# Optimization experiments

Hardware: AMD Instinct MI355X
Metric: run time of the kernel (lower is better)

The kernel has to match this reference:

```python
import jax, jax.numpy as jnp
import numpy as np

N = 100000       # num_nodes
E = 1600000      # num_edges (avg degree 16)
EL = 200000      # link-prediction edges
IN_C = 64
POS = 16
HID = 64
OUT = 32


def setup_inputs() -> dict:
    key = jax.random.key(0)
    ks = jax.random.split(key, 10)
    def glorot(k, shape):
        scale = 1.0 / np.sqrt(shape[0])
        return jax.random.uniform(k, shape, jnp.float32, -scale, scale)
    return {
        "x": jax.random.normal(ks[0], (N, IN_C), jnp.float32),
        "pos_emb": jax.random.normal(ks[1], (N, POS), jnp.float32),
        "W1": glorot(ks[2], (IN_C + POS, HID)),
        "b1": jnp.zeros((HID,), jnp.float32),
        "W2": glorot(ks[3], (HID, OUT)),
        "b2": jnp.zeros((OUT,), jnp.float32),
        "Wl": glorot(ks[4], (2 * OUT, 1)),
        "bl": jnp.zeros((1,), jnp.float32),
        "edge_index": jax.random.randint(ks[5], (2, E), 0, N, jnp.int32),
        "edge_label_index": jax.random.randint(ks[6], (2, EL), 0, N, jnp.int32),
    }


def reference(x, pos_emb, W1, b1, W2, b2, Wl, bl, edge_index, edge_label_index):
    n = x.shape[0]
    # GCNConv: add self-loops, symmetric deg^{-1/2} normalization (PyG defaults)
    loops = jnp.arange(n, dtype=edge_index.dtype)
    src = jnp.concatenate([edge_index[0], loops])  # [E+N]
    dst = jnp.concatenate([edge_index[1], loops])  # [E+N]
    deg = jax.ops.segment_sum(jnp.ones_like(dst, jnp.float32), dst, num_segments=n)
    dinv = jnp.where(deg > 0, jax.lax.rsqrt(jnp.maximum(deg, 1e-12)), 0.0)
    norm = dinv[src] * dinv[dst]  # [E+N]

    def gcn_conv(h, W, b):
        hw = h @ W                                    # [N, d_out] transform first
        msg = hw[src] * norm[:, None]                 # gather + normalize
        return jax.ops.segment_sum(msg, dst, num_segments=n) + b  # scatter-add

    h = jnp.concatenate([x, pos_emb], axis=1)         # [N, in+pos]
    h = jax.nn.relu(gcn_conv(h, W1, b1))              # dropout is eval no-op
    z = gcn_conv(h, W2, b2)                           # [N, out]

    s, d = edge_label_index[0], edge_label_index[1]
    zc = jnp.concatenate([z[s], z[d]], axis=1)        # [EL, 2*out]
    edge_pred = (zc @ Wl + bl)[:, 0]                  # [EL]
    return z, edge_pred
```

## Files before the change

kernel.cpp:

```cpp
#include <hip/hip_runtime.h>
#include <hip/hip_fp16.h>

#define NN 100000
#define NE 1600000
#define NEL 200000
#define TM 64

#define NBUCK 196
#define CAPB  10240
#define TPE   8192

typedef short s16x8 __attribute__((ext_vector_type(8)));
typedef float f32x4 __attribute__((ext_vector_type(4)));

__device__ __forceinline__ unsigned short bf16hi(float v) {
    unsigned u = __float_as_uint(v);
    return (unsigned short)((u + 0x7FFFu + ((u >> 16) & 1u)) >> 16);
}
__device__ __forceinline__ float bf16tof(unsigned short b) {
    return __uint_as_float(((unsigned)b) << 16);
}

__global__ __launch_bounds__(256) void k_part(const int* __restrict__ src,
                                              const int* __restrict__ dst,
                                              int* __restrict__ gcur,
                                              int* __restrict__ part) {
    __shared__ int hist[NBUCK];
    __shared__ int base[NBUCK];
    __shared__ int rk[NBUCK];
    int tid = threadIdx.x;
    for (int i = tid; i < NBUCK; i += 256) { hist[i] = 0; rk[i] = 0; }
    __syncthreads();
    int e0 = blockIdx.x * TPE;
    int e1 = min(e0 + TPE, NE);
    for (int e = e0 + tid; e < e1; e += 256)
        atomicAdd(&hist[dst[e] >> 9], 1);
    __syncthreads();
    for (int i = tid; i < NBUCK; i += 256)
        base[i] = i * CAPB + atomicAdd(&gcur[i], hist[i]);
    __syncthreads();
    for (int e = e0 + tid; e < e1; e += 256) {
        int d = dst[e];
        int s = src[e];
        int b = d >> 9;
        int r = atomicAdd(&rk[b], 1);
        part[base[b] + r] = ((d & 511) << 17) | s;
    }
}

__global__ __launch_bounds__(256) void k_build(const int* __restrict__ gcur,
                                               const int* __restrict__ part,
                                               int* __restrict__ csr,
                                               int* __restrict__ off,
                                               float* __restrict__ dinv) {
    __shared__ int cnts[256];
    __shared__ int hist[512];
    __shared__ int loff[512];
    __shared__ int ssum[256];
    __shared__ int csrbuf[CAPB];
    int b = blockIdx.x;
    int tid = threadIdx.x;
    cnts[tid] = (tid < NBUCK) ? gcur[tid] : 0;
    __syncthreads();
    for (int st = 1; st < 256; st <<= 1) {
        int tmp = (tid >= st) ? cnts[tid - st] : 0;
        __syncthreads();
        cnts[tid] += tmp;
        __syncthreads();
    }
    int obase = (b == 0) ? 0 : cnts[b - 1];
    int cnt = gcur[b];
    int pbase = b * CAPB;
    hist[tid] = 0; hist[tid + 256] = 0;
    __syncthreads();
    for (int i = tid; i < cnt; i += 256)
        atomicAdd(&hist[part[pbase + i] >> 17], 1);
    __syncthreads();
    int a0 = hist[2 * tid], a1 = hist[2 * tid + 1];
    int pairs = a0 + a1;
    ssum[tid] = pairs;
    __syncthreads();
    for (int st = 1; st < 256; st <<= 1) {
        int tmp = (tid >= st) ? ssum[tid - st] : 0;
        __syncthreads();
        ssum[tid] += tmp;
        __syncthreads();
    }
    int pexcl = ssum[tid] - pairs;
    loff[2 * tid] = pexcl;
    loff[2 * tid + 1] = pexcl + a0;
    __syncthreads();
    for (int i = tid; i < 512; i += 256) {
        int d = b * 512 + i;
        if (d < NN) {
            int c = hist[i];
            off[d] = obase + loff[i] + c;
            dinv[d] = rsqrtf((float)(c + 1));
        }
    }
    hist[tid] = 0; hist[tid + 256] = 0;
    __syncthreads();
    for (int i = tid; i < cnt; i += 256) {
        int rec = part[pbase + i];
        int dl = rec >> 17;
        int r = atomicAdd(&hist[dl], 1);
        csrbuf[loff[dl] + r] = rec & 0x1FFFF;
    }
    __syncthreads();
    for (int i = tid; i < cnt; i += 256)
        csr[obase + i] = csrbuf[i];
}

#define HW1_K 104
__global__ __launch_bounds__(256) void k_hw1(const float* __restrict__ x,
                                             const float* __restrict__ pos,
                                             const float* __restrict__ W1,
                                             const float* __restrict__ dinv,
                                             __half* __restrict__ hw1) {
    __shared__ unsigned short ahi[64 * HW1_K];
    __shared__ unsigned short alo[64 * HW1_K];
    __shared__ unsigned short bhi[64 * HW1_K];
    __shared__ unsigned short blo[64 * HW1_K];
    __shared__ float sdin[64];
    int tid = threadIdx.x;
    int nb = blockIdx.x * 64;
    for (int i = tid; i < 64 * 24; i += 256) {
        int r = i / 24, c = i - r * 24;
        ahi[r * HW1_K + 80 + c] = 0; alo[r * HW1_K + 80 + c] = 0;
        bhi[r * HW1_K + 80 + c] = 0; blo[r * HW1_K + 80 + c] = 0;
    }
    for (int i = tid; i < 64 * 64; i += 256) {
        int r = i >> 6, c = i & 63;
        int g = nb + r;
        float v = (g < NN) ? x[g * 64 + c] : 0.0f;
        unsigned short h = bf16hi(v);
        ahi[r * HW1_K + c] = h;
        alo[r * HW1_K + c] = bf16hi(v - bf16tof(h));
    }
    for (int i = tid; i < 64 * 16; i += 256) {
        int r = i >> 4, c = i & 15;
        int g = nb + r;
        float v = (g < NN) ? pos[g * 16 + c] : 0.0f;
        unsigned short h = bf16hi(v);
        ahi[r * HW1_K + 64 + c] = h;
        alo[r * HW1_K + 64 + c] = bf16hi(v - bf16tof(h));
    }
    for (int i = tid; i < 80 * 64; i += 256) {
        int k = i >> 6, c = i & 63;
        float v = W1[i];
        unsigned short h = bf16hi(v);
        bhi[c * HW1_K + k] = h;
        blo[c * HW1_K + k] = bf16hi(v - bf16tof(h));
    }
    for (int i = tid; i < 64; i += 256) {
        int g = nb + i;
        sdin[i] = (g < NN) ? dinv[g] : 0.0f;
    }
    __syncthreads();
    int wave = tid >> 6, lane = tid & 63;
    int frow = lane & 15, fq = lane >> 4;
    int r0 = wave * 16;
    int aoff = (r0 + frow) * HW1_K + fq * 8;
    s16x8 ah0 = *(s16x8*)&ahi[aoff];
    s16x8 ah1 = *(s16x8*)&ahi[aoff + 32];
    s16x8 ah2 = *(s16x8*)&ahi[aoff + 64];
    s16x8 al0 = *(s16x8*)&alo[aoff];
    s16x8 al1 = *(s16x8*)&alo[aoff + 32];
    s16x8 al2 = *(s16x8*)&alo[aoff + 64];
    f32x4 acc[4];
#pragma unroll
    for (int ct = 0; ct < 4; ++ct) {
        acc[ct] = (f32x4)(0.0f);
        int boff = (ct * 16 + frow) * HW1_K + fq * 8;
        s16x8 bh0 = *(s16x8*)&bhi[boff];
        s16x8 bh1 = *(s16x8*)&bhi[boff + 32];
        s16x8 bh2 = *(s16x8*)&bhi[boff + 64];
        s16x8 bl0 = *(s16x8*)&blo[boff];
        s16x8 bl1 = *(s16x8*)&blo[boff + 32];
        s16x8 bl2 = *(s16x8*)&blo[boff + 64];
        acc[ct] = __builtin_amdgcn_mfma_f32_16x16x32_bf16(ah0, bh0, acc[ct], 0, 0, 0);
        acc[ct] = __builtin_amdgcn_mfma_f32_16x16x32_bf16(ah1, bh1, acc[ct], 0, 0, 0);
        acc[ct] = __builtin_amdgcn_mfma_f32_16x16x32_bf16(ah2, bh2, acc[ct], 0, 0, 0);
        acc[ct] = __builtin_amdgcn_mfma_f32_16x16x32_bf16(ah0, bl0, acc[ct], 0, 0, 0);
        acc[ct] = __builtin_amdgcn_mfma_f32_16x16x32_bf16(ah1, bl1, acc[ct], 0, 0, 0);
        acc[ct] = __builtin_amdgcn_mfma_f32_16x16x32_bf16(ah2, bl2, acc[ct], 0, 0, 0);
        acc[ct] = __builtin_amdgcn_mfma_f32_16x16x32_bf16(al0, bh0, acc[ct], 0, 0, 0);
        acc[ct] = __builtin_amdgcn_mfma_f32_16x16x32_bf16(al1, bh1, acc[ct], 0, 0, 0);
        acc[ct] = __builtin_amdgcn_mfma_f32_16x16x32_bf16(al2, bh2, acc[ct], 0, 0, 0);
    }
#pragma unroll
    for (int ct = 0; ct < 4; ++ct) {
        int col = ct * 16 + frow;
#pragma unroll
        for (int i = 0; i < 4; ++i) {
            int r = r0 + fq * 4 + i;
            int g = nb + r;
            if (g < NN)
                hw1[g * 64 + col] = __float2half_rn(acc[ct][i] * sdin[r]);
        }
    }
}

__global__ __launch_bounds__(256) void k_gather1(const int* __restrict__ off,
                                                 const int* __restrict__ csr,
                                                 const float* __restrict__ dinv,
                                                 const __half* __restrict__ hw,
                                                 const float* __restrict__ b1,
                                                 const float* __restrict__ W2,
                                                 __half* __restrict__ hw2out) {
    __shared__ float sW2[64 * 32];
    __shared__ float h2row[4][64];
    int tid = threadIdx.x;
    for (int t = tid; t < 64 * 32; t += 256) sW2[t] = W2[t];
    int lane = tid & 63;
    int wave = tid >> 6;
    int d = blockIdx.x * 4 + wave;
    int start = (d == 0) ? 0 : off[d - 1];
    int end = off[d];
    start = __builtin_amdgcn_readfirstlane(start);
    end   = __builtin_amdgcn_readfirstlane(end);
    float dd = dinv[d];
    float hself = __half2float(hw[d * 64 + lane]);
    __syncthreads();
    float acc0 = 0.0f, acc1 = 0.0f, acc2 = 0.0f, acc3 = 0.0f;
    for (int e = start; e < end; e += 16) {
        int rem = end - e;
        int s0 = csr[e];
        int s1  = (rem > 1)  ? csr[e + 1]  : s0;
        int s2  = (rem > 2)  ? csr[e + 2]  : s0;
        int s3  = (rem > 3)  ? csr[e + 3]  : s0;
        int s4  = (rem > 4)  ? csr[e + 4]  : s0;
        int s5  = (rem > 5)  ? csr[e + 5]  : s0;
        int s6  = (rem > 6)  ? csr[e + 6]  : s0;
        int s7  = (rem > 7)  ? csr[e + 7]  : s0;
        int s8  = (rem > 8)  ? csr[e + 8]  : s0;
        int s9  = (rem > 9)  ? csr[e + 9]  : s0;
        int s10 = (rem > 10) ? csr[e + 10] : s0;
        int s11 = (rem > 11) ? csr[e + 11] : s0;
        int s12 = (rem > 12) ? csr[e + 12] : s0;
        int s13 = (rem > 13) ? csr[e + 13] : s0;
        int s14 = (rem > 14) ? csr[e + 14] : s0;
        int s15 = (rem > 15) ? csr[e + 15] : s0;
        float g0  = __half2float(hw[s0  * 64 + lane]);
        float g1  = __half2float(hw[s1  * 64 + lane]);
        float g2  = __half2float(hw[s2  * 64 + lane]);
        float g3  = __half2float(hw[s3  * 64 + lane]);
        float g4  = __half2float(hw[s4  * 64 + lane]);
        float g5  = __half2float(hw[s5  * 64 + lane]);
        float g6  = __half2float(hw[s6  * 64 + lane]);
        float g7  = __half2float(hw[s7  * 64 + lane]);
        float g8  = __half2float(hw[s8  * 64 + lane]);
        float g9  = __half2float(hw[s9  * 64 + lane]);
        float g10 = __half2float(hw[s10 * 64 + lane]);
        float g11 = __half2float(hw[s11 * 64 + lane]);
        float g12 = __half2float(hw[s12 * 64 + lane]);
        float g13 = __half2float(hw[s13 * 64 + lane]);
        float g14 = __half2float(hw[s14 * 64 + lane]);
        float g15 = __half2float(hw[s15 * 64 + lane]);
        int inv = 16 - rem;
        if (inv < 0) inv = 0;
        acc0 += g0;  acc1 += g1;  acc2 += g2;  acc3 += g3;
        acc0 += g4;  acc1 += g5;  acc2 += g6;  acc3 += g7;
        acc0 += g8;  acc1 += g9;  acc2 += g10; acc3 += g11;
        acc0 += g12; acc1 += g13; acc2 += g14; acc3 += g15;
        acc3 = fmaf(-(float)inv, g0, acc3);
    }
    float v = fmaxf(b1[lane] + dd * (((acc0 + acc1) + (acc2 + acc3)) + hself), 0.0f);
    h2row[wave][lane] = v;
    int j = lane & 31;
    int half = lane >> 5;
    float sum = 0.0f;
#pragma unroll
    for (int k = 0; k < 32; ++k) {
        int kk = half * 32 + k;
        sum += h2row[wave][kk] * sW2[kk * 32 + j];
    }
    sum += __shfl_xor(sum, 32, 64);
    if (half == 0)
        hw2out[d * 32 + j] = __float2half_rn(sum * dd);
}

__global__ __launch_bounds__(256) void k_gather2(const int* __restrict__ off,
                                                 const int* __restrict__ csr,
                                                 const float* __restrict__ dinv,
                                                 const __half* __restrict__ hw,
                                                 const float* __restrict__ b2,
                                                 const float* __restrict__ Wl,
                                                 float* __restrict__ outz,
                                                 float* __restrict__ uu,
                                                 float* __restrict__ vv) {
    int lane = threadIdx.x & 63;
    int half = lane >> 5;
    int j = lane & 31;
    int wave = threadIdx.x >> 6;
    int d = blockIdx.x * 4 + wave;
    int start = (d == 0) ? 0 : off[d - 1];
    int end = off[d];
    start = __builtin_amdgcn_readfirstlane(start);
    end   = __builtin_amdgcn_readfirstlane(end);
    float dd = dinv[d];
    float hself = __half2float(hw[d * 32 + j]);
    float accA = 0.0f, accB = 0.0f, accC = 0.0f, accD = 0.0f;
    for (int e = start; e < end; e += 16) {
        int rem = end - e;
        int s0 = csr[e];
        int i1 = e + half;
        int sA = (half      < rem) ? csr[i1]      : s0;
        int sB = (half + 2  < rem) ? csr[i1 + 2]  : s0;
        int sC = (half + 4  < rem) ? csr[i1 + 4]  : s0;
        int sD = (half + 6  < rem) ? csr[i1 + 6]  : s0;
        int sE = (half + 8  < rem) ? csr[i1 + 8]  : s0;
        int sF = (half + 10 < rem) ? csr[i1 + 10] : s0;
        int sG = (half + 12 < rem) ? csr[i1 + 12] : s0;
        int sH = (half + 14 < rem) ? csr[i1 + 14] : s0;
        float gA = __half2float(hw[sA * 32 + j]);
        float gB = __half2float(hw[sB * 32 + j]);
        float gC = __half2float(hw[sC * 32 + j]);
        float gD = __half2float(hw[sD * 32 + j]);
        float gE = __half2float(hw[sE * 32 + j]);
        float gF = __half2float(hw[sF * 32 + j]);
        float gG = __half2float(hw[sG * 32 + j]);
        float gH = __half2float(hw[sH * 32 + j]);
        int nv = (rem - half + 1) >> 1;
        if (nv > 8) nv = 8;
        int inv = 8 - nv;
        accA += gA; accB += gB; accC += gC; accD += gD;
        accA += gE; accB += gF; accC += gG; accD += gH;
        accD = fmaf(-(float)inv, gH, accD);
    }
    float acc = (accA + accB) + (accC + accD);
    acc += __shfl(acc, lane ^ 32, 64);
    float z = b2[j] + dd * (acc + hself);
    if (half == 0)
        outz[d * 32 + j] = z;
    float p0 = z * Wl[j];
    float p1 = z * Wl[32 + j];
    p0 += __shfl_xor(p0, 1, 64);  p1 += __shfl_xor(p1, 1, 64);
    p0 += __shfl_xor(p0, 2, 64);  p1 += __shfl_xor(p1, 2, 64);
    p0 += __shfl_xor(p0, 4, 64);  p1 += __shfl_xor(p1, 4, 64);
    p0 += __shfl_xor(p0, 8, 64);  p1 += __shfl_xor(p1, 8, 64);
    p0 += __shfl_xor(p0, 16, 64); p1 += __shfl_xor(p1, 16, 64);
    if (lane == 0) { uu[d] = p0; vv[d] = p1; }
}

__global__ __launch_bounds__(256) void k_linkpred(const int* __restrict__ sidx,
                                                  const int* __restrict__ didx,
                                                  const float* __restrict__ uu,
                                                  const float* __restrict__ vv,
                                                  const float* __restrict__ bl,
                                                  float* __restrict__ pred) {
    int e = blockIdx.x * 256 + threadIdx.x;
    if (e < NEL)
        pred[e] = uu[sidx[e]] + vv[didx[e]] + bl[0];
}

extern "C" void kernel_launch(void* const* d_in, const int* in_sizes, int n_in,
                              void* d_out, int out_size, void* d_ws, size_t ws_size,
                              hipStream_t stream) {
    const float* x    = (const float*)d_in[0];
    const float* pos  = (const float*)d_in[1];
    const float* W1   = (const float*)d_in[2];
    const float* b1   = (const float*)d_in[3];
    const float* W2   = (const float*)d_in[4];
    const float* b2   = (const float*)d_in[5];
    const float* Wl   = (const float*)d_in[6];
    const float* bl   = (const float*)d_in[7];
    const int*   ei   = (const int*)d_in[8];
    const int*   eli  = (const int*)d_in[9];
    const int* src  = ei;
    const int* dst  = ei + NE;
    const int* lsrc = eli;
    const int* ldst = eli + NEL;

    float* out_z    = (float*)d_out;
    float* out_pred = (float*)d_out + NN * 32;

    float*  dinv  = (float*)d_ws;
    int*    off   = (int*)(dinv + NN);
    int*    gcur  = off + NN;
    int*    csr   = gcur + NBUCK;
    __half* hw1   = (__half*)(csr + NE);
    int*    part  = (int*)hw1;
    __half* hw2   = hw1 + NN * 64;
    float*  uu    = (float*)(hw2 + NN * 32);
    float*  vv    = uu + NN;

    hipMemsetAsync(gcur, 0, NBUCK * sizeof(int), stream);
    k_part<<<(NE + TPE - 1) / TPE, 256, 0, stream>>>(src, dst, gcur, part);
    k_build<<<NBUCK, 256, 0, stream>>>(gcur, part, csr, off, dinv);

    k_hw1<<<(NN + TM - 1) / TM, 256, 0, stream>>>(x, pos, W1, dinv, hw1);

    k_gather1<<<NN / 4, 256, 0, stream>>>(off, csr, dinv, hw1, b1, W2, hw2);

    k_gather2<<<NN / 4, 256, 0, stream>>>(off, csr, dinv, hw2, b2, Wl,
                                          out_z, uu, vv);

    k_linkpred<<<(NEL + 255) / 256, 256, 0, stream>>>(lsrc, ldst, uu, vv, bl,
                                                      out_pred);
}
```

Measured before the change: 280.2 us.

## Fuse CSR partition and build kernels via grid-wide atomic barrier

Merges the partition and bucket-build kernels into one 196-block kernel that uses a global atomic counter as a grid barrier, removing one launch and its inter-kernel gap. Shared memory is unioned between the two phases. It also drops staging W2 into shared memory in the first gather kernel and reads it directly from global, which removes a block-wide sync. The grid barrier depends on all 196 blocks being co-resident, which holds on a GPU with enough CUs but would deadlock otherwise.

```diff
diff --git a/kernel.cpp b/kernel.cpp
--- a/kernel.cpp
+++ b/kernel.cpp
@@ -9,6 +9,7 @@
 #define NBUCK 196
 #define CAPB  10240
 #define TPE   8192
+#define NPART 196
 
 typedef short s16x8 __attribute__((ext_vector_type(8)));
 typedef float f32x4 __attribute__((ext_vector_type(4)));
@@ -21,94 +22,96 @@
     return __uint_as_float(((unsigned)b) << 16);
 }
 
-__global__ __launch_bounds__(256) void k_part(const int* __restrict__ src,
-                                              const int* __restrict__ dst,
-                                              int* __restrict__ gcur,
-                                              int* __restrict__ part) {
-    __shared__ int hist[NBUCK];
-    __shared__ int base[NBUCK];
-    __shared__ int rk[NBUCK];
+union CsrSmem {
+    struct { int hist[NBUCK], base[NBUCK], rk[NBUCK]; } p;
+    struct { int cnts[256], hist[512], loff[512], ssum[256], csrbuf[CAPB]; } b;
+};
+__global__ __launch_bounds__(256) void k_csr(const int* __restrict__ src,
+                                             const int* __restrict__ dst,
+                                             int* __restrict__ gcur,
+                                             int* __restrict__ bar,
+                                             int* __restrict__ part,
+                                             int* __restrict__ csr,
+                                             int* __restrict__ off,
+                                             float* __restrict__ dinv) {
+    __shared__ CsrSmem sm;
     int tid = threadIdx.x;
-    for (int i = tid; i < NBUCK; i += 256) { hist[i] = 0; rk[i] = 0; }
-    __syncthreads();
-    int e0 = blockIdx.x * TPE;
+    int b = blockIdx.x;
+    for (int i = tid; i < NBUCK; i += 256) { sm.p.hist[i] = 0; sm.p.rk[i] = 0; }
+    __syncthreads();
+    int e0 = b * TPE;
     int e1 = min(e0 + TPE, NE);
     for (int e = e0 + tid; e < e1; e += 256)
-        atomicAdd(&hist[dst[e] >> 9], 1);
+        atomicAdd(&sm.p.hist[dst[e] >> 9], 1);
     __syncthreads();
     for (int i = tid; i < NBUCK; i += 256)
-        base[i] = i * CAPB + atomicAdd(&gcur[i], hist[i]);
+        sm.p.base[i] = i * CAPB + atomicAdd(&gcur[i], sm.p.hist[i]);
     __syncthreads();
     for (int e = e0 + tid; e < e1; e += 256) {
         int d = dst[e];
         int s = src[e];
-        int b = d >> 9;
-        int r = atomicAdd(&rk[b], 1);
-        part[base[b] + r] = ((d & 511) << 17) | s;
-    }
-}
-
-__global__ __launch_bounds__(256) void k_build(const int* __restrict__ gcur,
-                                               const int* __restrict__ part,
-                                               int* __restrict__ csr,
-                                               int* __restrict__ off,
-                                               float* __restrict__ dinv) {
-    __shared__ int cnts[256];
-    __shared__ int hist[512];
-    __shared__ int loff[512];
-    __shared__ int ssum[256];
-    __shared__ int csrbuf[CAPB];
-    int b = blockIdx.x;
-    int tid = threadIdx.x;
-    cnts[tid] = (tid < NBUCK) ? gcur[tid] : 0;
+        int bk = d >> 9;
+        int r = atomicAdd(&sm.p.rk[bk], 1);
+        part[sm.p.base[bk] + r] = ((d & 511) << 17) | s;
+    }
+    __syncthreads();
+    if (tid == 0) {
+        __threadfence();
+        __hip_atomic_fetch_add(bar, 1, __ATOMIC_RELEASE, __HIP_MEMORY_SCOPE_AGENT);
+        while (__hip_atomic_load(bar, __ATOMIC_ACQUIRE, __HIP_MEMORY_SCOPE_AGENT) < NPART)
+            __builtin_amdgcn_s_sleep(16);
+        __threadfence();
+    }
+    __syncthreads();
+    sm.b.cnts[tid] = (tid < NBUCK) ? gcur[tid] : 0;
     __syncthreads();
     for (int st = 1; st < 256; st <<= 1) {
-        int tmp = (tid >= st) ? cnts[tid - st] : 0;
+        int tmp = (tid >= st) ? sm.b.cnts[tid - st] : 0;
         __syncthreads();
-        cnts[tid] += tmp;
+        sm.b.cnts[tid] += tmp;
         __syncthreads();
     }
-    int obase = (b == 0) ? 0 : cnts[b - 1];
+    int obase = (b == 0) ? 0 : sm.b.cnts[b - 1];
     int cnt = gcur[b];
     int pbase = b * CAPB;
-    hist[tid] = 0; hist[tid + 256] = 0;
+    sm.b.hist[tid] = 0; sm.b.hist[tid + 256] = 0;
     __syncthreads();
     for (int i = tid; i < cnt; i += 256)
-        atomicAdd(&hist[part[pbase + i] >> 17], 1);
-    __syncthreads();
-    int a0 = hist[2 * tid], a1 = hist[2 * tid + 1];
+        atomicAdd(&sm.b.hist[part[pbase + i] >> 17], 1);
+    __syncthreads();
+    int a0 = sm.b.hist[2 * tid], a1 = sm.b.hist[2 * tid + 1];
     int pairs = a0 + a1;
-    ssum[tid] = pairs;
+    sm.b.ssum[tid] = pairs;
     __syncthreads();
     for (int st = 1; st < 256; st <<= 1) {
-        int tmp = (tid >= st) ? ssum[tid - st] : 0;
+        int tmp = (tid >= st) ? sm.b.ssum[tid - st] : 0;
         __syncthreads();
-        ssum[tid] += tmp;
+        sm.b.ssum[tid] += tmp;
         __syncthreads();
     }
-    int pexcl = ssum[tid] - pairs;
-    loff[2 * tid] = pexcl;
-    loff[2 * tid + 1] = pexcl + a0;
+    int pexcl = sm.b.ssum[tid] - pairs;
+    sm.b.loff[2 * tid] = pexcl;
+    sm.b.loff[2 * tid + 1] = pexcl + a0;
     __syncthreads();
     for (int i = tid; i < 512; i += 256) {
         int d = b * 512 + i;
         if (d < NN) {
-            int c = hist[i];
-            off[d] = obase + loff[i] + c;
+            int c = sm.b.hist[i];
+            off[d] = obase + sm.b.loff[i] + c;
             dinv[d] = rsqrtf((float)(c + 1));
         }
     }
-    hist[tid] = 0; hist[tid + 256] = 0;
+    sm.b.hist[tid] = 0; sm.b.hist[tid + 256] = 0;
     __syncthreads();
     for (int i = tid; i < cnt; i += 256) {
         int rec = part[pbase + i];
         int dl = rec >> 17;
-        int r = atomicAdd(&hist[dl], 1);
-        csrbuf[loff[dl] + r] = rec & 0x1FFFF;
+        int r = atomicAdd(&sm.b.hist[dl], 1);
+        sm.b.csrbuf[sm.b.loff[dl] + r] = rec & 0x1FFFF;
     }
     __syncthreads();
     for (int i = tid; i < cnt; i += 256)
-        csr[obase + i] = csrbuf[i];
+        csr[obase + i] = sm.b.csrbuf[i];
 }
 
 #define HW1_K 104
@@ -208,10 +211,8 @@
                                                  const float* __restrict__ b1,
                                                  const float* __restrict__ W2,
                                                  __half* __restrict__ hw2out) {
-    __shared__ float sW2[64 * 32];
     __shared__ float h2row[4][64];
     int tid = threadIdx.x;
-    for (int t = tid; t < 64 * 32; t += 256) sW2[t] = W2[t];
     int lane = tid & 63;
     int wave = tid >> 6;
     int d = blockIdx.x * 4 + wave;
@@ -221,7 +222,6 @@
     end   = __builtin_amdgcn_readfirstlane(end);
     float dd = dinv[d];
     float hself = __half2float(hw[d * 64 + lane]);
-    __syncthreads();
     float acc0 = 0.0f, acc1 = 0.0f, acc2 = 0.0f, acc3 = 0.0f;
     for (int e = start; e < end; e += 16) {
         int rem = end - e;
@@ -273,7 +273,7 @@
 #pragma unroll
     for (int k = 0; k < 32; ++k) {
         int kk = half * 32 + k;
-        sum += h2row[wave][kk] * sW2[kk * 32 + j];
+        sum += h2row[wave][kk] * W2[kk * 32 + j];
     }
     sum += __shfl_xor(sum, 32, 64);
     if (half == 0)
@@ -378,16 +378,17 @@
     float*  dinv  = (float*)d_ws;
     int*    off   = (int*)(dinv + NN);
     int*    gcur  = off + NN;
-    int*    csr   = gcur + NBUCK;
+    int*    bar   = gcur + NBUCK;
+    int*    csr   = bar + 1;
     __half* hw1   = (__half*)(csr + NE);
     int*    part  = (int*)hw1;
     __half* hw2   = hw1 + NN * 64;
     float*  uu    = (float*)(hw2 + NN * 32);
     float*  vv    = uu + NN;
 
-    hipMemsetAsync(gcur, 0, NBUCK * sizeof(int), stream);
-    k_part<<<(NE + TPE - 1) / TPE, 256, 0, stream>>>(src, dst, gcur, part);
-    k_build<<<NBUCK, 256, 0, stream>>>(gcur, part, csr, off, dinv);
+    hipMemsetAsync(gcur, 0, (NBUCK + 1) * sizeof(int), stream);
+
+    k_csr<<<NPART, 256, 0, stream>>>(src, dst, gcur, bar, part, csr, off, dinv);
 
     k_hw1<<<(NN + TM - 1) / TM, 256, 0, stream>>>(x, pos, W1, dinv, hw1);
 
```

Result: slower. 299.7 us (+6.9%).
